# Kernel tuning notes

Hardware: AMD Instinct MI355X
Metric: run time of the kernel (lower is better)

## Reference

```python
import jax, jax.numpy as jnp
import numpy as np

NUM_HEADS = 12


def setup_inputs() -> dict:
    key = jax.random.key(0)
    k1, k2, k3 = jax.random.split(key, 3)
    B, N, C = 16, 1024, 768
    x = jax.random.normal(k1, (B, N, C), dtype=jnp.float32)
    w_qkv = jax.random.normal(k2, (C, 3 * C), dtype=jnp.float32) * (C ** -0.5)
    w_proj = jax.random.normal(k3, (C, C), dtype=jnp.float32) * (C ** -0.5)
    b_proj = jnp.zeros((C,), dtype=jnp.float32)
    return {"x": x, "w_qkv": w_qkv, "w_proj": w_proj, "b_proj": b_proj}


def reference(x, w_qkv, w_proj, b_proj):
    B, N, C = x.shape
    H = NUM_HEADS
    d = C // H
    scale = d ** -0.5
    # QKV projection (no bias, qkv_bias=False)
    qkv = jnp.einsum('bnc,cf->bnf', x, w_qkv)            # [B, N, 3C]
    qkv = qkv.reshape(B, N, 3, H, d).transpose(2, 0, 3, 1, 4)  # [3, B, H, N, d]
    q, k, v = qkv[0], qkv[1], qkv[2]
    attn = jnp.einsum('bhnd,bhmd->bhnm', q, k) * scale   # [B, H, N, N]
    attn = jax.nn.softmax(attn, axis=-1)
    out = jnp.einsum('bhnm,bhmd->bhnd', attn, v)          # [B, H, N, d]
    # Faithful to source: reshape [B,H,N,d] -> [B,N,H*d] WITHOUT head transpose
    out = out.reshape(B, N, H * d)
    return jnp.einsum('bnc,cf->bnf', out, w_proj) + b_proj
```

## Files before the change

kernel.cpp:

```cpp
#include <hip/hip_runtime.h>
#include <math.h>
#include <cstddef>
#include <cstdint>


typedef _Float16 half8 __attribute__((ext_vector_type(8)));
typedef _Float16 half4 __attribute__((ext_vector_type(4)));
typedef float f32x4 __attribute__((ext_vector_type(4)));

__device__ __forceinline__ void async_ld16(const void* src, void* lds) {
  __builtin_amdgcn_global_load_lds(
      (const __attribute__((address_space(1))) unsigned int*)src,
      (__attribute__((address_space(3))) unsigned int*)lds, 16, 0, 0);
}

__device__ __forceinline__ f32x4 mfma16(half8 a, half8 b, f32x4 c) {
  return __builtin_amdgcn_mfma_f32_16x16x32_f16(a, b, c, 0, 0, 0);
}

__global__ __launch_bounds__(256) void conv_split(const float* __restrict__ src,
                                                  _Float16* __restrict__ hi,
                                                  _Float16* __restrict__ lo,
                                                  int n8) {
  for (int i = blockIdx.x * blockDim.x + threadIdx.x; i < n8;
       i += gridDim.x * blockDim.x) {
    const float4 f0 = ((const float4*)src)[i * 2];
    const float4 f1 = ((const float4*)src)[i * 2 + 1];
    const float x[8] = {f0.x, f0.y, f0.z, f0.w, f1.x, f1.y, f1.z, f1.w};
    half8 h, l;
#pragma unroll
    for (int j = 0; j < 8; ++j) {
      const _Float16 hv = (_Float16)x[j];
      h[j] = hv;
      l[j] = (_Float16)(x[j] - (float)hv);
    }
    ((half8*)hi)[i] = h;
    ((half8*)lo)[i] = l;
  }
}

__global__ __launch_bounds__(256) void conv_wT(const float* __restrict__ W,
                                               _Float16* __restrict__ Th,
                                               _Float16* __restrict__ Tl,
                                               int K, int N) {
  __shared__ float T[64][65];
  const int n0 = blockIdx.x * 64, k0 = blockIdx.y * 64;
  const int t = threadIdx.x, r = t >> 2, c4 = t & 3;
#pragma unroll
  for (int q = 0; q < 4; ++q) {
    const float4 v = *reinterpret_cast<const float4*>(
        &W[(size_t)(k0 + r) * N + n0 + c4 * 16 + q * 4]);
    T[r][c4 * 16 + q * 4 + 0] = v.x;
    T[r][c4 * 16 + q * 4 + 1] = v.y;
    T[r][c4 * 16 + q * 4 + 2] = v.z;
    T[r][c4 * 16 + q * 4 + 3] = v.w;
  }
  __syncthreads();
  half8 h0, h1, l0, l1;
#pragma unroll
  for (int j = 0; j < 8; ++j) {
    const float x0 = T[c4 * 16 + j][r];
    const _Float16 hv0 = (_Float16)x0;
    h0[j] = hv0; l0[j] = (_Float16)(x0 - (float)hv0);
    const float x1 = T[c4 * 16 + 8 + j][r];
    const _Float16 hv1 = (_Float16)x1;
    h1[j] = hv1; l1[j] = (_Float16)(x1 - (float)hv1);
  }
  const size_t ob = (size_t)(n0 + r) * K + k0 + c4 * 16;
  *(half8*)&Th[ob] = h0;
  *(half8*)&Th[ob + 8] = h1;
  *(half8*)&Tl[ob] = l0;
  *(half8*)&Tl[ob + 8] = l1;
}

template <bool HAS_BIAS>
__global__ __launch_bounds__(256, 2) void gemm_split(
    const _Float16* __restrict__ Ah, const _Float16* __restrict__ Al,
    const _Float16* __restrict__ Bh, const _Float16* __restrict__ Bl,
    const float* __restrict__ bias, float* __restrict__ C,
    int M, int N, int K) {
  __shared__ _Float16 AsH[128 * 64], AsL[128 * 64], BsH[128 * 64], BsL[128 * 64];
  const int tid = threadIdx.x;
  const int w = tid >> 6, l = tid & 63;
  const int kl = l & 15, lgrp = l >> 4;
  const int rl = l >> 3, cl = l & 7;
  const int bm = blockIdx.y * 128, bn = blockIdx.x * 128;
  const int wm = (w & 1) * 64, wn = (w >> 1) * 64;

  f32x4 acc[4][4];
#pragma unroll
  for (int m = 0; m < 4; ++m)
#pragma unroll
    for (int n = 0; n < 4; ++n) acc[m][n] = f32x4{0.f, 0.f, 0.f, 0.f};

  for (int k0 = 0; k0 < K; k0 += 64) {
    __syncthreads();
#pragma unroll
    for (int j = 0; j < 4; ++j) {
      const int rloc = w * 32 + j * 8 + rl;
      const size_t koff = (size_t)k0 + ((cl ^ (rloc & 7)) << 3);
      const int ldsb = (w * 32 + j * 8) * 64;
      async_ld16(Ah + (size_t)(bm + rloc) * K + koff, &AsH[ldsb]);
      async_ld16(Al + (size_t)(bm + rloc) * K + koff, &AsL[ldsb]);
      async_ld16(Bh + (size_t)(bn + rloc) * K + koff, &BsH[ldsb]);
      async_ld16(Bl + (size_t)(bn + rloc) * K + koff, &BsL[ldsb]);
    }
    asm volatile("s_waitcnt vmcnt(0)" ::: "memory");
    __syncthreads();

#pragma unroll
    for (int ks = 0; ks < 2; ++ks) {
      half8 ah[4], al[4], bh[4], bl[4];
#pragma unroll
      for (int m = 0; m < 4; ++m) {
        const int row = wm + m * 16 + kl;
        const int off = row * 64 + (((ks * 4 + lgrp) ^ (row & 7)) << 3);
        ah[m] = *(const half8*)&AsH[off];
        al[m] = *(const half8*)&AsL[off];
      }
#pragma unroll
      for (int n = 0; n < 4; ++n) {
        const int row = wn + n * 16 + kl;
        const int off = row * 64 + (((ks * 4 + lgrp) ^ (row & 7)) << 3);
        bh[n] = *(const half8*)&BsH[off];
        bl[n] = *(const half8*)&BsL[off];
      }
#pragma unroll
      for (int m = 0; m < 4; ++m)
#pragma unroll
        for (int n = 0; n < 4; ++n) {
          acc[m][n] = mfma16(ah[m], bh[n], acc[m][n]);
          acc[m][n] = mfma16(al[m], bh[n], acc[m][n]);
          acc[m][n] = mfma16(ah[m], bl[n], acc[m][n]);
        }
    }
  }

  float bv[4];
  if (HAS_BIAS) {
#pragma unroll
    for (int n = 0; n < 4; ++n) bv[n] = bias[bn + wn + n * 16 + kl];
  }
#pragma unroll
  for (int m = 0; m < 4; ++m)
#pragma unroll
    for (int r = 0; r < 4; ++r) {
      const int row = bm + wm + m * 16 + lgrp * 4 + r;
#pragma unroll
      for (int n = 0; n < 4; ++n) {
        float v = acc[m][n][r];
        if (HAS_BIAS) v += bv[n];
        C[(size_t)row * N + bn + wn + n * 16 + kl] = v;
      }
    }
}

__global__ __launch_bounds__(256) void prep_kv(float* __restrict__ qkv) {
  constexpr int N = 1024, C3 = 2304;
  const int nt = blockIdx.x, h = blockIdx.y, b = blockIdx.z;
  const int t = threadIdx.x;
  __shared__ float Vls[64 * 65];

  const int r = t >> 2, dc = t & 3;
  const size_t rowf = (size_t)(b * N + nt * 64 + r) * C3 + h * 64;

  float kx[16], vx[16];
#pragma unroll
  for (int q = 0; q < 4; ++q) {
    const float4 kv = *reinterpret_cast<const float4*>(&qkv[rowf + 768 + dc * 16 + q * 4]);
    kx[q * 4 + 0] = kv.x; kx[q * 4 + 1] = kv.y; kx[q * 4 + 2] = kv.z; kx[q * 4 + 3] = kv.w;
    const float4 vv = *reinterpret_cast<const float4*>(&qkv[rowf + 1536 + dc * 16 + q * 4]);
    vx[q * 4 + 0] = vv.x; vx[q * 4 + 1] = vv.y; vx[q * 4 + 2] = vv.z; vx[q * 4 + 3] = vv.w;
  }
#pragma unroll
  for (int i = 0; i < 16; ++i) Vls[r * 65 + dc * 16 + i] = vx[i];
  __syncthreads();

  {
    char* base = (char*)qkv + (rowf + 768) * 4;
    half8 h0, h1, l0, l1;
#pragma unroll
    for (int i = 0; i < 8; ++i) {
      const _Float16 hi = (_Float16)kx[i];
      h0[i] = hi; l0[i] = (_Float16)(kx[i] - (float)hi);
      const _Float16 hi2 = (_Float16)kx[i + 8];
      h1[i] = hi2; l1[i] = (_Float16)(kx[i + 8] - (float)hi2);
    }
    *(half8*)(base + dc * 32) = h0;
    *(half8*)(base + dc * 32 + 16) = h1;
    *(half8*)(base + 128 + dc * 32) = l0;
    *(half8*)(base + 128 + dc * 32 + 16) = l1;
  }

#pragma unroll
  for (int p = 0; p < 2; ++p) {
    const int dd = p * 32 + (t >> 3), nc = t & 7;
    half8 hv, lv;
#pragma unroll
    for (int j = 0; j < 8; ++j) {
      const int pos = nc * 8 + j;
      const int kap = ((pos & 3) << 4) | (pos >> 2);
      const float x = Vls[kap * 65 + dd];
      const _Float16 hi = (_Float16)x;
      hv[j] = hi; lv[j] = (_Float16)(x - (float)hi);
    }
    char* vb = (char*)qkv + ((size_t)(b * N + nt * 64 + dd) * C3 + h * 64 + 1536) * 4;
    *(half8*)(vb + nc * 16) = hv;
    *(half8*)(vb + 128 + nc * 16) = lv;
  }
}

__global__ __launch_bounds__(256, 2) void attn_mfma(const float* __restrict__ qkv,
                                                    _Float16* __restrict__ ahi,
                                                    _Float16* __restrict__ alo) {
  constexpr int N = 1024, H = 12, C3 = 2304;
  const int blk = blockIdx.x;
  const int xcd = blk & 7;
  const int slot = blk >> 3;
  const int qt = slot & 7;
  const int bh = xcd * 24 + (slot >> 3);
  const int h = bh % H;
  const int b = bh / H;

  const int tid = threadIdx.x;
  const int w = tid >> 6, l = tid & 63;
  const int kl = l & 15, lgrp = l >> 4;

  __shared__ _Float16 Khi[64 * 64], Klo[64 * 64], Vhi[64 * 64], Vlo[64 * 64];
  __shared__ _Float16 Phi[128 * 64], Plo[128 * 64];

  const int q0 = qt * 128;

  half8 qhi[2][2], qlo[2][2];
#pragma unroll
  for (int qs = 0; qs < 2; ++qs)
#pragma unroll
    for (int ks = 0; ks < 2; ++ks) {
      const float* qp = qkv + (size_t)(b * N + q0 + w * 32 + qs * 16 + kl) * C3 +
                        h * 64 + ks * 32 + lgrp * 8;
      const float4 f0 = *reinterpret_cast<const float4*>(qp);
      const float4 f1 = *reinterpret_cast<const float4*>(qp + 4);
      const float x[8] = {f0.x, f0.y, f0.z, f0.w, f1.x, f1.y, f1.z, f1.w};
#pragma unroll
      for (int j = 0; j < 8; ++j) {
        const float xs = x[j] * 0.125f;
        const _Float16 hi = (_Float16)xs;
        qhi[qs][ks][j] = hi;
        qlo[qs][ks][j] = (_Float16)(xs - (float)hi);
      }
    }

  f32x4 o[2][4];
  float plsum[2][4];
#pragma unroll
  for (int qs = 0; qs < 2; ++qs)
#pragma unroll
    for (int i = 0; i < 4; ++i) {
      plsum[qs][i] = 0.f;
      o[qs][i] = f32x4{0.f, 0.f, 0.f, 0.f};
    }

  const char* qkvB = (const char*)qkv;
  const int rl = l >> 3, cl = l & 7;

  auto stageK = [&](int kb) {
#pragma unroll
    for (int i = 0; i < 2; ++i) {
      const int row = w * 16 + i * 8 + rl;
      const size_t rb = ((size_t)(b * N + kb * 64 + row) * C3 + h * 64) * 4;
      const int sw = (cl ^ (row & 7)) * 16;
      const char* kc = qkvB + rb + 768 * 4 + sw;
      const int lo_ = (w * 16 + i * 8) * 64;
      async_ld16(kc, &Khi[lo_]);
      async_ld16(kc + 128, &Klo[lo_]);
    }
  };
  auto stageV = [&](int kb) {
#pragma unroll
    for (int i = 0; i < 2; ++i) {
      const int row = w * 16 + i * 8 + rl;
      const size_t rb = ((size_t)(b * N + kb * 64 + row) * C3 + h * 64) * 4;
      const int sw = (cl ^ (row & 7)) * 16;
      const char* vc = qkvB + rb + 1536 * 4 + sw;
      const int lo_ = (w * 16 + i * 8) * 64;
      async_ld16(vc, &Vhi[lo_]);
      async_ld16(vc + 128, &Vlo[lo_]);
    }
  };

  stageK(0);
  stageV(0);
  asm volatile("s_waitcnt vmcnt(0)" ::: "memory");
  __builtin_amdgcn_s_barrier();

  for (int kb = 0; kb < 16; ++kb) {
    f32x4 s[2][4];
#pragma unroll
    for (int qs = 0; qs < 2; ++qs)
#pragma unroll
      for (int kt = 0; kt < 4; ++kt) s[qs][kt] = f32x4{0.f, 0.f, 0.f, 0.f};

#pragma unroll
    for (int kt = 0; kt < 4; ++kt)
#pragma unroll
      for (int ks = 0; ks < 2; ++ks) {
        const int rowb = kt * 16 + kl;
        const int off = rowb * 64 + (((ks * 4 + lgrp) ^ (rowb & 7)) << 3);
        const half8 bh_ = *(const half8*)&Khi[off];
        const half8 bl_ = *(const half8*)&Klo[off];
#pragma unroll
        for (int qs = 0; qs < 2; ++qs) {
          s[qs][kt] = mfma16(qhi[qs][ks], bh_, s[qs][kt]);
          s[qs][kt] = mfma16(qlo[qs][ks], bh_, s[qs][kt]);
          s[qs][kt] = mfma16(qhi[qs][ks], bl_, s[qs][kt]);
        }
      }

    asm volatile("s_waitcnt vmcnt(0)" ::: "memory");
    __builtin_amdgcn_s_barrier();
    if (kb < 15) stageK(kb + 1);

#pragma unroll
    for (int qs = 0; qs < 2; ++qs)
#pragma unroll
      for (int r = 0; r < 4; ++r) {
        const int prow = w * 32 + qs * 16 + lgrp * 4 + r;
        float ps = 0.f;
        half4 ph4, pl4;
#pragma unroll
        for (int kt = 0; kt < 4; ++kt) {
          const float p = __expf(s[qs][kt][r]);
          ps += p;
          const _Float16 ph = (_Float16)p;
          ph4[kt] = ph;
          pl4[kt] = (_Float16)(p - (float)ph);
        }
        *(half4*)&Phi[prow * 64 + kl * 4] = ph4;
        *(half4*)&Plo[prow * 64 + kl * 4] = pl4;
        plsum[qs][r] += ps;
      }

#pragma unroll
    for (int ks = 0; ks < 2; ++ks) {
      half8 pah[2], pal[2];
#pragma unroll
      for (int qs = 0; qs < 2; ++qs) {
        const int off = (w * 32 + qs * 16 + kl) * 64 + ks * 32 + lgrp * 8;
        pah[qs] = *(const half8*)&Phi[off];
        pal[qs] = *(const half8*)&Plo[off];
      }
#pragma unroll
      for (int dt = 0; dt < 4; ++dt) {
        const int rowv = dt * 16 + kl;
        const int off = rowv * 64 + (((ks * 4 + lgrp) ^ (rowv & 7)) << 3);
        const half8 vh = *(const half8*)&Vhi[off];
        const half8 vl = *(const half8*)&Vlo[off];
#pragma unroll
        for (int qs = 0; qs < 2; ++qs) {
          o[qs][dt] = mfma16(pah[qs], vh, o[qs][dt]);
          o[qs][dt] = mfma16(pah[qs], vl, o[qs][dt]);
          o[qs][dt] = mfma16(pal[qs], vh, o[qs][dt]);
        }
      }
    }

    __builtin_amdgcn_s_barrier();
    if (kb < 15) {
      stageV(kb + 1);
      asm volatile("s_waitcnt vmcnt(4)" ::: "memory");
    } else {
      asm volatile("s_waitcnt vmcnt(0)" ::: "memory");
    }
    __builtin_amdgcn_s_barrier();
  }

#pragma unroll
  for (int qs = 0; qs < 2; ++qs)
#pragma unroll
    for (int r = 0; r < 4; ++r) {
      float lsum = plsum[qs][r];
#pragma unroll
      for (int ofs = 1; ofs < 16; ofs <<= 1) lsum += __shfl_xor(lsum, ofs);
      const float inv = 1.f / lsum;
      const int qg = q0 + w * 32 + qs * 16 + lgrp * 4 + r;
      const size_t ob = ((size_t)(b * H + h) * N + qg) * 64;
#pragma unroll
      for (int dt = 0; dt < 4; ++dt) {
        const float v = o[qs][dt][r] * inv;
        const _Float16 hv = (_Float16)v;
        ahi[ob + dt * 16 + kl] = hv;
        alo[ob + dt * 16 + kl] = (_Float16)(v - (float)hv);
      }
    }
}

extern "C" void kernel_launch(void* const* d_in, const int* in_sizes, int n_in,
                              void* d_out, int out_size, void* d_ws,
                              size_t ws_size, hipStream_t stream) {
  const float* x = (const float*)d_in[0];
  const float* w_qkv = (const float*)d_in[1];
  const float* w_proj = (const float*)d_in[2];
  const float* b_proj = (const float*)d_in[3];
  float* out = (float*)d_out;

  constexpr int M = 16 * 1024;
  constexpr int C = 768;
  constexpr int C3 = 2304;

  char* wsp = (char*)d_ws;
  float* qkv = (float*)wsp;
  _Float16* xhi = (_Float16*)(wsp + (size_t)M * C3 * 4);
  _Float16* xlo = xhi + (size_t)M * C;
  _Float16* wqh = xlo + (size_t)M * C;
  _Float16* wql = wqh + (size_t)C3 * C;
  _Float16* wph = wql + (size_t)C3 * C;
  _Float16* wpl = wph + (size_t)C * C;
  _Float16* ahi = xhi;
  _Float16* alo = xlo;

  conv_split<<<2048, 256, 0, stream>>>(x, xhi, xlo, M * C / 8);
  conv_wT<<<dim3(C3 / 64, C / 64), 256, 0, stream>>>(w_qkv, wqh, wql, C, C3);
  conv_wT<<<dim3(C / 64, C / 64), 256, 0, stream>>>(w_proj, wph, wpl, C, C);

  gemm_split<false><<<dim3(C3 / 128, M / 128), 256, 0, stream>>>(
      xhi, xlo, wqh, wql, nullptr, qkv, M, C3, C);

  prep_kv<<<dim3(16, 12, 16), 256, 0, stream>>>(qkv);

  attn_mfma<<<1536, 256, 0, stream>>>(qkv, ahi, alo);

  gemm_split<true><<<dim3(C / 128, M / 128), 256, 0, stream>>>(
      ahi, alo, wph, wpl, b_proj, out, M, C, C);
}
```

Measured before the change: 537.6 us.

## Double-buffer GEMM LDS tiles and swizzle attention P buffer

The split-precision GEMM drops from one 64-wide K tile per iteration to two ping-pong LDS buffers of 32-wide K tiles. The next tile's async global-to-LDS loads are issued before the MFMAs on the current tile, so loads overlap compute and one barrier per step is removed. Separately, the attention kernel's P hi/lo LDS writes and reads now use an XOR swizzle on row bits to reduce bank conflicts. The GEMM no longer has an explicit vmcnt wait before its barrier, so correctness relies on the barrier lowering waiting for the LDS-DMA loads.

```diff
diff --git a/kernel.cpp b/kernel.cpp
--- a/kernel.cpp
+++ b/kernel.cpp
@@ -79,11 +79,12 @@
     const _Float16* __restrict__ Bh, const _Float16* __restrict__ Bl,
     const float* __restrict__ bias, float* __restrict__ C,
     int M, int N, int K) {
-  __shared__ _Float16 AsH[128 * 64], AsL[128 * 64], BsH[128 * 64], BsL[128 * 64];
+  __shared__ _Float16 AsH[2][128 * 32], AsL[2][128 * 32];
+  __shared__ _Float16 BsH[2][128 * 32], BsL[2][128 * 32];
   const int tid = threadIdx.x;
   const int w = tid >> 6, l = tid & 63;
   const int kl = l & 15, lgrp = l >> 4;
-  const int rl = l >> 3, cl = l & 7;
+  const int rl4 = l >> 2, cl4 = l & 3;
   const int bm = blockIdx.y * 128, bn = blockIdx.x * 128;
   const int wm = (w & 1) * 64, wn = (w >> 1) * 64;
 
@@ -93,47 +94,55 @@
 #pragma unroll
     for (int n = 0; n < 4; ++n) acc[m][n] = f32x4{0.f, 0.f, 0.f, 0.f};
 
-  for (int k0 = 0; k0 < K; k0 += 64) {
+  const int nt = K >> 5;
+
+  auto stage = [&](int t, int buf) {
+    const int k0 = t << 5;
+#pragma unroll
+    for (int j = 0; j < 2; ++j) {
+      const int row = w * 32 + j * 16 + rl4;
+      const size_t koff = (size_t)k0 + ((cl4 ^ ((row >> 1) & 3)) << 3);
+      const int ldsb = (w * 32 + j * 16) * 32;
+      async_ld16(Ah + (size_t)(bm + row) * K + koff, &AsH[buf][ldsb]);
+      async_ld16(Al + (size_t)(bm + row) * K + koff, &AsL[buf][ldsb]);
+      async_ld16(Bh + (size_t)(bn + row) * K + koff, &BsH[buf][ldsb]);
+      async_ld16(Bl + (size_t)(bn + row) * K + koff, &BsL[buf][ldsb]);
+    }
+  };
+
+  stage(0, 0);
+  __syncthreads();
+
+  int cur = 0;
+  for (int t = 0; t < nt; ++t) {
+    if (t + 1 < nt) stage(t + 1, cur ^ 1);
+
+    half8 ah[4], al[4], bh[4], bl[4];
+#pragma unroll
+    for (int m = 0; m < 4; ++m) {
+      const int row = wm + m * 16 + kl;
+      const int off = row * 32 + ((lgrp ^ ((row >> 1) & 3)) << 3);
+      ah[m] = *(const half8*)&AsH[cur][off];
+      al[m] = *(const half8*)&AsL[cur][off];
+    }
+#pragma unroll
+    for (int n = 0; n < 4; ++n) {
+      const int row = wn + n * 16 + kl;
+      const int off = row * 32 + ((lgrp ^ ((row >> 1) & 3)) << 3);
+      bh[n] = *(const half8*)&BsH[cur][off];
+      bl[n] = *(const half8*)&BsL[cur][off];
+    }
+#pragma unroll
+    for (int m = 0; m < 4; ++m)
+#pragma unroll
+      for (int n = 0; n < 4; ++n) {
+        acc[m][n] = mfma16(ah[m], bh[n], acc[m][n]);
+        acc[m][n] = mfma16(al[m], bh[n], acc[m][n]);
+        acc[m][n] = mfma16(ah[m], bl[n], acc[m][n]);
+      }
+
     __syncthreads();
-#pragma unroll
-    for (int j = 0; j < 4; ++j) {
-      const int rloc = w * 32 + j * 8 + rl;
-      const size_t koff = (size_t)k0 + ((cl ^ (rloc & 7)) << 3);
-      const int ldsb = (w * 32 + j * 8) * 64;
-      async_ld16(Ah + (size_t)(bm + rloc) * K + koff, &AsH[ldsb]);
-      async_ld16(Al + (size_t)(bm + rloc) * K + koff, &AsL[ldsb]);
-      async_ld16(Bh + (size_t)(bn + rloc) * K + koff, &BsH[ldsb]);
-      async_ld16(Bl + (size_t)(bn + rloc) * K + koff, &BsL[ldsb]);
-    }
-    asm volatile("s_waitcnt vmcnt(0)" ::: "memory");
-    __syncthreads();
-
-#pragma unroll
-    for (int ks = 0; ks < 2; ++ks) {
-      half8 ah[4], al[4], bh[4], bl[4];
-#pragma unroll
-      for (int m = 0; m < 4; ++m) {
-        const int row = wm + m * 16 + kl;
-        const int off = row * 64 + (((ks * 4 + lgrp) ^ (row & 7)) << 3);
-        ah[m] = *(const half8*)&AsH[off];
-        al[m] = *(const half8*)&AsL[off];
-      }
-#pragma unroll
-      for (int n = 0; n < 4; ++n) {
-        const int row = wn + n * 16 + kl;
-        const int off = row * 64 + (((ks * 4 + lgrp) ^ (row & 7)) << 3);
-        bh[n] = *(const half8*)&BsH[off];
-        bl[n] = *(const half8*)&BsL[off];
-      }
-#pragma unroll
-      for (int m = 0; m < 4; ++m)
-#pragma unroll
-        for (int n = 0; n < 4; ++n) {
-          acc[m][n] = mfma16(ah[m], bh[n], acc[m][n]);
-          acc[m][n] = mfma16(al[m], bh[n], acc[m][n]);
-          acc[m][n] = mfma16(ah[m], bl[n], acc[m][n]);
-        }
-    }
+    cur ^= 1;
   }
 
   float bv[4];
@@ -325,6 +334,7 @@
 #pragma unroll
       for (int r = 0; r < 4; ++r) {
         const int prow = w * 32 + qs * 16 + lgrp * 4 + r;
+        const int swz = (prow & 7) << 3;
         float ps = 0.f;
         half4 ph4, pl4;
 #pragma unroll
@@ -335,8 +345,8 @@
           ph4[kt] = ph;
           pl4[kt] = (_Float16)(p - (float)ph);
         }
-        *(half4*)&Phi[prow * 64 + kl * 4] = ph4;
-        *(half4*)&Plo[prow * 64 + kl * 4] = pl4;
+        *(half4*)&Phi[prow * 64 + ((kl * 4) ^ swz)] = ph4;
+        *(half4*)&Plo[prow * 64 + ((kl * 4) ^ swz)] = pl4;
         plsum[qs][r] += ps;
       }
 
@@ -345,7 +355,8 @@
       half8 pah[2], pal[2];
 #pragma unroll
       for (int qs = 0; qs < 2; ++qs) {
-        const int off = (w * 32 + qs * 16 + kl) * 64 + ks * 32 + lgrp * 8;
+        const int prow = w * 32 + qs * 16 + kl;
+        const int off = prow * 64 + ((ks * 32 + lgrp * 8) ^ ((prow & 7) << 3));
         pah[qs] = *(const half8*)&Phi[off];
         pal[qs] = *(const half8*)&Plo[off];
       }
```

New measurement: 546.1 us. Within noise of the previous version (+1.6%).
